# Optimization experiments

Hardware: AMD Instinct MI355X
Metric: run time of the kernel (lower is better)

The kernel has to match this reference:

```python
import jax, jax.numpy as jnp
import numpy as np

# irreps_in = 64x0e + 32x1o + 16x2e ; output of FCTP = 64x0e
MULS = (64, 32, 16)
LS = (0, 1, 2)
IRR_DIM = sum(m * (2 * l + 1) for m, l in zip(MULS, LS))  # 240
HID = 64   # hidden_fea_len
Z = 64     # z_fea_len
N = 50000
# e3nn path normalization ('element', normalization='component'):
# each l x l -> 0e path weight = sqrt(ir_out.dim / sum_paths(mul1*mul2)) = 1/sqrt(64^2+32^2+16^2)
PATH_NORM = 1.0 / np.sqrt(sum(m * m for m in MULS))


def _split(t):
    # slice flat irrep vector into per-irrep [N, mul, 2l+1] blocks
    blocks, i = [], 0
    for m, l in zip(MULS, LS):
        d = 2 * l + 1
        blocks.append(t[:, i:i + m * d].reshape(-1, m, d))
        i += m * d
    return blocks


def _fctp(t, W0, W1, W2):
    # FullyConnectedTensorProduct(irr, irr, '64x0e'):
    # for each l, CG w3j(l,l,0)[m,m'] = delta_{mm'} / sqrt(2l+1),
    # out[n,k] = sum_l pw_l * sum_{u,v} W_l[u,v,k] * <x_l[n,u,:], x_l[n,v,:]> / sqrt(2l+1)
    out = 0.0
    for x, W, l in zip(_split(t), (W0, W1, W2), LS):
        d = 2 * l + 1
        dot = jnp.einsum('num,nvm->nuv', x, x) * (PATH_NORM / np.sqrt(d))
        out = out + jnp.einsum('nuv,uvk->nk', dot, W)
    return out


def _mlp(h, A1, b1, A2, b2, A3, b3):
    h = jax.nn.silu(h @ A1.T + b1)
    h = jax.nn.silu(h @ A2.T + b2)
    return h @ A3.T + b3


def setup_inputs() -> dict:
    key = jax.random.key(0)
    ks = jax.random.split(key, 8)
    return {
        'tensor_in': jax.random.normal(ks[0], (N, IRR_DIM), jnp.float32),
        # FCTP weights (e3nn init: standard normal; normalization lives in PATH_NORM)
        'W0': jax.random.normal(ks[1], (64, 64, HID), jnp.float32),
        'W1': jax.random.normal(ks[2], (32, 32, HID), jnp.float32),
        'W2': jax.random.normal(ks[3], (16, 16, HID), jnp.float32),
        # nn.Linear params (y = x @ A.T + b)
        'A1': jax.random.normal(ks[4], (HID, HID), jnp.float32) / np.sqrt(HID),
        'b1': jnp.zeros((HID,), jnp.float32),
        'A2': jax.random.normal(ks[5], (Z, HID), jnp.float32) / np.sqrt(HID),
        'b2': jnp.zeros((Z,), jnp.float32),
        'A3': jax.random.normal(ks[6], (Z, Z), jnp.float32) / np.sqrt(Z),
        'b3': jnp.zeros((Z,), jnp.float32),
    }


def reference(tensor_in, W0, W1, W2, A1, b1, A2, b2, A3, b3):
    def fwd(t):
        return _mlp(_fctp(t, W0, W1, W2), A1, b1, A2, b2, A3, b3)

    # x = MLP(FCTP(t, t)); y = d(sum(x))/dt  (autograd.grad with ones grad_outputs)
    x, vjp_fn = jax.vjp(fwd, tensor_in)
    y = vjp_fn(jnp.ones_like(x))[0]
    return (x, y)
```

## Files before the change

### kernel.cpp

```cpp
#include <hip/hip_runtime.h>
#include <math.h>
#include <utility>


typedef short bf8 __attribute__((ext_vector_type(8)));
typedef float f4 __attribute__((ext_vector_type(4)));

constexpr int IRR = 240;

constexpr int NP = 2880;

struct PTab { short u[NP]; short v[NP]; signed char l[NP]; };
constexpr PTab build_ptab() {
    PTab t{}; int p = 0;
    for (int u = 0; u < 64; u++) for (int v = u; v < 64; v++) { t.u[p]=(short)u; t.v[p]=(short)v; t.l[p]=0; p++; }
    while (p < 2112) { t.l[p] = -1; p++; }
    for (int u = 0; u < 32; u++) for (int v = u; v < 32; v++) { t.u[p]=(short)u; t.v[p]=(short)v; t.l[p]=1; p++; }
    while (p < 2688) { t.l[p] = -1; p++; }
    for (int u = 0; u < 16; u++) for (int v = u; v < 16; v++) { t.u[p]=(short)u; t.v[p]=(short)v; t.l[p]=2; p++; }
    while (p < NP)   { t.l[p] = -1; p++; }
    return t;
}
constexpr PTab PT = build_ptab();

constexpr size_t B_WTF = 0;
constexpr size_t B_WB  = (size_t)64 * NP * 2;
constexpr size_t B_A1T = B_WB + (size_t)5376 * 64 * 2;
constexpr size_t B_A2T = B_A1T + 16384;
constexpr size_t B_A3T = B_A2T + 16384;
constexpr size_t B_DG2 = B_A3T + 16384;
constexpr size_t B_H   = B_DG2 + 256;

__device__ __forceinline__ unsigned short f2bf(float x) {
    unsigned int u = __float_as_uint(x);
    return (unsigned short)((u + 0x7fffu + ((u >> 16) & 1u)) >> 16);
}
__device__ __forceinline__ unsigned pack2(float a, float b) {
    unsigned ua = __float_as_uint(a) + 0x8000u;
    unsigned ub = __float_as_uint(b) + 0x8000u;
    return __builtin_amdgcn_perm(ub, ua, 0x07060302u);
}

__global__ void prep_kernel(const float* __restrict__ W0, const float* __restrict__ W1,
                            const float* __restrict__ W2, const float* __restrict__ A1,
                            const float* __restrict__ A2, const float* __restrict__ A3,
                            unsigned short* __restrict__ wtf, unsigned short* __restrict__ wb,
                            float* __restrict__ a1t, float* __restrict__ a2t,
                            float* __restrict__ a3t, float* __restrict__ dg2)
{
    int idx = blockIdx.x * blockDim.x + threadIdx.x;
    const double c0 = 1.0 / sqrt(5376.0);
    const double cl_[3] = { c0, c0 / sqrt(3.0), c0 / sqrt(5.0) };
    if (idx < 64 * NP) {
        int c = idx / NP, p = idx - c * NP;
        unsigned short val = 0;
        int l = -1, local = 0, mul = 0;
        if (p < 2112)      { local = p;        if (local < 2080) { l = 0; mul = 64; } }
        else if (p < 2688) { local = p - 2112; if (local < 528)  { l = 1; mul = 32; } }
        else               { local = p - 2688; if (local < 136)  { l = 2; mul = 16; } }
        if (l >= 0) {
            int u = 0;
            while ((u + 1) * mul - (u + 1) * u / 2 <= local) u++;
            int v = u + (local - (u * mul - u * (u - 1) / 2));
            const float* W = (l == 0) ? W0 : (l == 1) ? W1 : W2;
            float wv = W[(u * mul + v) * 64 + c];
            if (u != v) wv += W[(v * mul + u) * 64 + c];
            val = f2bf((float)(cl_[l] * wv));
        }
        wtf[(size_t)c * NP + p] = val;
        return;
    }
    idx -= 64 * NP;
    if (idx < 5376 * 64) {
        int pair = idx >> 6, c = idx & 63;
        int l, w, v, mul;
        if (pair < 4096)      { l = 0; mul = 64; w = pair >> 6;          v = pair & 63; }
        else if (pair < 5120) { l = 1; mul = 32; w = (pair - 4096) >> 5; v = (pair - 4096) & 31; }
        else                  { l = 2; mul = 16; w = (pair - 5120) >> 4; v = (pair - 5120) & 15; }
        const float* W = (l == 0) ? W0 : (l == 1) ? W1 : W2;
        float val;
        if (v == w) val = (float)(2.0 * cl_[l]) * W[(w * mul + w) * 64 + c];
        else        val = (float)cl_[l] * (W[(w * mul + v) * 64 + c] + W[(v * mul + w) * 64 + c]);
        wb[(size_t)pair * 64 + c] = f2bf(val);
        return;
    }
    idx -= 5376 * 64;
    if (idx < 3 * 4096) {
        int m = idx >> 12, e = idx & 4095;
        int j = e >> 6, k = e & 63;
        const float* A = (m == 0) ? A1 : (m == 1) ? A2 : A3;
        float* dst     = (m == 0) ? a1t : (m == 1) ? a2t : a3t;
        dst[j * 64 + k] = A[k * 64 + j];
        return;
    }
    idx -= 3 * 4096;
    if (idx < 64) {
        float s = 0.f;
        for (int k = 0; k < 64; k++) s += A3[k * 64 + idx];
        dg2[idx] = s;
    }
}

template <int P, int NX>
__device__ __forceinline__ float pval(const float (&x)[NX]) {
    constexpr int l = PT.l[P];
    if constexpr (l < 0) {
        return 0.f;
    } else if constexpr (l == 0) {
        return x[PT.u[P]] * x[PT.v[P]];
    } else if constexpr (l == 1) {
        constexpr int u = 3 * PT.u[P], v = 3 * PT.v[P];
        return x[u] * x[v] + x[u + 1] * x[v + 1] + x[u + 2] * x[v + 2];
    } else {
        constexpr int u = 5 * PT.u[P], v = 5 * PT.v[P];
        return x[u] * x[v] + x[u + 1] * x[v + 1] + x[u + 2] * x[v + 2]
             + x[u + 3] * x[v + 3] + x[u + 4] * x[v + 4];
    }
}

template <int CH, int O, int NX>
__device__ __forceinline__ void p_octet(const float (&xr)[NX],
        unsigned short (&Pb)[64][64], int lane)
{
    uint4 w;
    w.x = pack2(pval<CH * 64 + O * 8 + 0, NX>(xr), pval<CH * 64 + O * 8 + 1, NX>(xr));
    w.y = pack2(pval<CH * 64 + O * 8 + 2, NX>(xr), pval<CH * 64 + O * 8 + 3, NX>(xr));
    w.z = pack2(pval<CH * 64 + O * 8 + 4, NX>(xr), pval<CH * 64 + O * 8 + 5, NX>(xr));
    w.w = pack2(pval<CH * 64 + O * 8 + 6, NX>(xr), pval<CH * 64 + O * 8 + 7, NX>(xr));
    *(uint4*)&Pb[lane][(O ^ (lane & 7)) * 8] = w;
}

template <int CH, int NX, int... Os>
__device__ __forceinline__ void p_octets(std::integer_sequence<int, Os...>,
        const float (&xr)[NX], unsigned short (&Pb)[64][64], int lane)
{
    (p_octet<CH, Os, NX>(xr, Pb, lane), ...);
}

template <int CH>
__device__ __forceinline__ void load_bfrags(bf8 (&b)[8],
        const unsigned short* __restrict__ wtf, int l15, int quad)
{
    #pragma unroll
    for (int ct = 0; ct < 4; ++ct)
        #pragma unroll
        for (int ks = 0; ks < 2; ++ks)
            b[ct * 2 + ks] = *(const bf8*)(wtf + (size_t)(16 * ct + l15) * NP
                                           + CH * 64 + ks * 32 + quad * 8);
}

template <int CH, int NX>
__device__ __forceinline__ void fwd_body(const float (&xr)[NX],
        unsigned short (&Pb)[64][64], f4 (&acc)[4][4], const bf8 (&bc)[8],
        int lane, int l15, int quad)
{
    p_octets<CH, NX>(std::make_integer_sequence<int, 8>{}, xr, Pb, lane);
    asm volatile("s_waitcnt lgkmcnt(0)" ::: "memory");
    bf8 a[4][2];
    #pragma unroll
    for (int rt = 0; rt < 4; ++rt) {
        int row = 16 * rt + l15;
        #pragma unroll
        for (int ks = 0; ks < 2; ++ks)
            a[rt][ks] = *(const bf8*)&Pb[row][((ks * 4 + quad) ^ (row & 7)) * 8];
    }
    #pragma unroll
    for (int ct = 0; ct < 4; ++ct)
        #pragma unroll
        for (int ks = 0; ks < 2; ++ks)
            #pragma unroll
            for (int rt = 0; rt < 4; ++rt)
                acc[rt][ct] = __builtin_amdgcn_mfma_f32_16x16x32_bf16(
                                  a[rt][ks], bc[ct * 2 + ks], acc[rt][ct], 0, 0, 0);
    asm volatile("" ::: "memory");
}

template <int B, int N, int I, int NX>
__device__ __forceinline__ void fwd_rec(const float (&xr)[NX],
        unsigned short (&Pb)[64][64], const unsigned short* __restrict__ wtf,
        f4 (&acc)[4][4], bf8 (&bc)[8], int lane, int l15, int quad)
{
    if constexpr (I + 1 < N) {
        bf8 bn[8];
        load_bfrags<B + I + 1>(bn, wtf, l15, quad);
        fwd_body<B + I, NX>(xr, Pb, acc, bc, lane, l15, quad);
        fwd_rec<B, N, I + 1, NX>(xr, Pb, wtf, acc, bn, lane, l15, quad);
    } else {
        fwd_body<B + I, NX>(xr, Pb, acc, bc, lane, l15, quad);
    }
}

template <int B, int N, int NX>
__device__ __forceinline__ void fwd_run_pf(const float (&xr)[NX],
        unsigned short (&Pb)[64][64], const unsigned short* __restrict__ wtf,
        f4 (&acc)[4][4], int lane, int l15, int quad)
{
    bf8 b0[8];
    load_bfrags<B>(b0, wtf, l15, quad);
    fwd_rec<B, N, 0, NX>(xr, Pb, wtf, acc, b0, lane, l15, quad);
}

__global__ __launch_bounds__(256) void fctp_fwd4(const float* __restrict__ tin,
        const unsigned short* __restrict__ wtf, float* __restrict__ h, int n)
{
    __shared__ unsigned short Pb[4][64][64];
    const int tid = threadIdx.x;
    const int wv = tid >> 6;
    const int lane = tid & 63;
    const int l15 = lane & 15, quad = lane >> 4;
    const int s0 = blockIdx.x * 64;
    const int s = s0 + lane;
    const int sld = (s < n) ? s : (n - 1);
    const float* xrow = tin + (size_t)sld * IRR;
    f4 acc[4][4];
    #pragma unroll
    for (int rt = 0; rt < 4; ++rt)
        #pragma unroll
        for (int ct = 0; ct < 4; ++ct) acc[rt][ct] = (f4){0.f, 0.f, 0.f, 0.f};

    if (wv == 0) {
        float x0[64];
        #pragma unroll
        for (int q = 0; q < 16; ++q) *(float4*)&x0[4 * q] = *(const float4*)(xrow + 4 * q);
        fwd_run_pf<0, 17>(x0, Pb[0], wtf, acc, lane, l15, quad);
    } else if (wv == 1) {
        float x0[64];
        #pragma unroll
        for (int q = 0; q < 16; ++q) *(float4*)&x0[4 * q] = *(const float4*)(xrow + 4 * q);
        fwd_run_pf<17, 16>(x0, Pb[1], wtf, acc, lane, l15, quad);
    } else if (wv == 2) {
        float x1[96];
        #pragma unroll
        for (int q = 0; q < 24; ++q) *(float4*)&x1[4 * q] = *(const float4*)(xrow + 64 + 4 * q);
        fwd_run_pf<33, 9>(x1, Pb[2], wtf, acc, lane, l15, quad);
    } else {
        float x2[80];
        #pragma unroll
        for (int q = 0; q < 20; ++q) *(float4*)&x2[4 * q] = *(const float4*)(xrow + 160 + 4 * q);
        fwd_run_pf<42, 3>(x2, Pb[3], wtf, acc, lane, l15, quad);
    }

    float* red = (float*)Pb;
    #pragma unroll
    for (int rt = 0; rt < 4; ++rt) {
        __syncthreads();
        #pragma unroll
        for (int ct = 0; ct < 4; ++ct) {
            float4 v = make_float4(acc[rt][ct][0], acc[rt][ct][1], acc[rt][ct][2], acc[rt][ct][3]);
            *(float4*)&red[(size_t)(wv * 64 + lane) * 20 + ct * 4] = v;
        }
        __syncthreads();
        float4 sum = make_float4(0.f, 0.f, 0.f, 0.f);
        #pragma unroll
        for (int w = 0; w < 4; ++w) {
            float4 v = *(const float4*)&red[(size_t)(w * 64 + lane) * 20 + wv * 4];
            sum.x += v.x; sum.y += v.y; sum.z += v.z; sum.w += v.w;
        }
        #pragma unroll
        for (int r = 0; r < 4; ++r) {
            int row = s0 + 16 * rt + 4 * quad + r;
            if (row < n) h[(size_t)row * 64 + 16 * wv + l15] = (&sum.x)[r];
        }
    }
}

__device__ __forceinline__ void load_awb(int ch, const unsigned short* __restrict__ wb,
        bf8 (&a)[8], int l15, int quad)
{
    #pragma unroll
    for (int rt = 0; rt < 4; ++rt)
        #pragma unroll
        for (int ks = 0; ks < 2; ++ks)
            a[rt * 2 + ks] = *(const bf8*)(wb + (size_t)(ch * 64 + 16 * rt + l15) * 64
                                           + ks * 32 + quad * 8);
}

__device__ __forceinline__ float l0_chunk(const bf8 (&a)[8], const bf8 (&bh)[4][2],
        const float (&xr)[64], int quad)
{
    float p0 = 0.f, p1 = 0.f, p2 = 0.f, p3 = 0.f;
    #pragma unroll
    for (int rt = 0; rt < 4; ++rt) {
        f4 dpR[4];
        #pragma unroll
        for (int ct = 0; ct < 4; ++ct) dpR[ct] = (f4){0.f, 0.f, 0.f, 0.f};
        #pragma unroll
        for (int ks = 0; ks < 2; ++ks)
            #pragma unroll
            for (int ct = 0; ct < 4; ++ct)
                dpR[ct] = __builtin_amdgcn_mfma_f32_16x16x32_bf16(
                              a[rt * 2 + ks], bh[ct][ks], dpR[ct], 0, 0, 0);
        #pragma unroll
        for (int r = 0; r < 4; ++r) {
            p0 += dpR[0][r] * xr[ 0 + rt * 4 + r];
            p1 += dpR[1][r] * xr[16 + rt * 4 + r];
            p2 += dpR[2][r] * xr[32 + rt * 4 + r];
            p3 += dpR[3][r] * xr[48 + rt * 4 + r];
        }
    }
    p0 += __shfl_xor(p0, 16); p0 += __shfl_xor(p0, 32);
    p1 += __shfl_xor(p1, 16); p1 += __shfl_xor(p1, 32);
    p2 += __shfl_xor(p2, 16); p2 += __shfl_xor(p2, 32);
    p3 += __shfl_xor(p3, 16); p3 += __shfl_xor(p3, 32);
    return (quad == 0) ? p0 : (quad == 1) ? p1 : (quad == 2) ? p2 : p3;
}

__global__ __launch_bounds__(256) void fctp_bwd_l0(const float* __restrict__ tin,
        const unsigned short* __restrict__ wb, const float* __restrict__ dh,
        float* __restrict__ y, int n)
{
    __shared__ __align__(16) unsigned char smem[64 * 68 * 4];
    float (*x0t)[68] = (float (*)[68])smem;
    unsigned short (*dhb)[64] = (unsigned short (*)[64])smem;

    const int tid  = threadIdx.x;
    const int wv   = tid >> 6;
    const int lane = tid & 63;
    const int l15 = lane & 15, quad = lane >> 4;
    const int s0 = blockIdx.x * 64;
    const int s = s0 + lane;
    const int sld = (s < n) ? s : (n - 1);
    const bool act = s < n;
    const float* xrow = tin + (size_t)sld * IRR;

    #pragma unroll
    for (int q = 0; q < 4; ++q)
        *(float4*)&x0t[lane][16 * wv + 4 * q] = *(const float4*)(xrow + 16 * wv + 4 * q);
    __syncthreads();
    float xr[64];
    #pragma unroll
    for (int ct = 0; ct < 4; ++ct)
        #pragma unroll
        for (int rt = 0; rt < 4; ++rt)
            *(float4*)&xr[ct * 16 + rt * 4] =
                *(const float4*)&x0t[16 * ct + l15][16 * rt + 4 * quad];
    __syncthreads();
    {
        const float* dhp = dh + (size_t)sld * 64;
        #pragma unroll
        for (int oo = 0; oo < 2; ++oo) {
            int o = 2 * wv + oo;
            float4 f0 = *(const float4*)(dhp + 8 * o);
            float4 f1 = *(const float4*)(dhp + 8 * o + 4);
            uint4 w = make_uint4(pack2(f0.x, f0.y), pack2(f0.z, f0.w),
                                 pack2(f1.x, f1.y), pack2(f1.z, f1.w));
            *(uint4*)&dhb[lane][(o ^ (lane & 7)) * 8] = w;
        }
    }
    __syncthreads();
    bf8 bh[4][2];
    #pragma unroll
    for (int ct = 0; ct < 4; ++ct) {
        int row = 16 * ct + l15;
        #pragma unroll
        for (int ks = 0; ks < 2; ++ks)
            bh[ct][ks] = *(const bf8*)&dhb[row][((ks * 4 + quad) ^ (row & 7)) * 8];
    }

    const int cbase = blockIdx.y * 16 + wv * 4;
    bf8 aA[8], aB[8];
    float res[4];
    load_awb(cbase + 0, wb, aA, l15, quad);
    load_awb(cbase + 1, wb, aB, l15, quad);
    res[0] = l0_chunk(aA, bh, xr, quad);
    load_awb(cbase + 2, wb, aA, l15, quad);
    res[1] = l0_chunk(aB, bh, xr, quad);
    load_awb(cbase + 3, wb, aB, l15, quad);
    res[2] = l0_chunk(aA, bh, xr, quad);
    res[3] = l0_chunk(aB, bh, xr, quad);
    if (act)
        *(float4*)&y[(size_t)s * IRR + cbase] = make_float4(res[0], res[1], res[2], res[3]);
}

__device__ __forceinline__ void bwd_mm(int ch, const unsigned short* __restrict__ wb,
        const bf8 (&bh)[4][2], float (*dPb)[68],
        int lane, int l15, int quad)
{
    f4 dp[4][4];
    #pragma unroll
    for (int rt = 0; rt < 4; ++rt)
        #pragma unroll
        for (int ct = 0; ct < 4; ++ct) dp[rt][ct] = (f4){0.f, 0.f, 0.f, 0.f};
    #pragma unroll
    for (int rt = 0; rt < 4; ++rt) {
        #pragma unroll
        for (int ks = 0; ks < 2; ++ks) {
            bf8 a = *(const bf8*)(wb + (size_t)(ch * 64 + 16 * rt + l15) * 64 + ks * 32 + quad * 8);
            #pragma unroll
            for (int ct = 0; ct < 4; ++ct)
                dp[rt][ct] = __builtin_amdgcn_mfma_f32_16x16x32_bf16(a, bh[ct][ks], dp[rt][ct], 0, 0, 0);
        }
    }
    #pragma unroll
    for (int rt = 0; rt < 4; ++rt)
        #pragma unroll
        for (int ct = 0; ct < 4; ++ct) {
            float4 v = make_float4(dp[rt][ct][0], dp[rt][ct][1], dp[rt][ct][2], dp[rt][ct][3]);
            *(float4*)&dPb[16 * ct + l15][16 * rt + 4 * quad] = v;
        }
    asm volatile("s_waitcnt lgkmcnt(0)" ::: "memory");
}

__global__ __launch_bounds__(256) void fctp_bwd_l12(const float* __restrict__ tin,
        const unsigned short* __restrict__ wb, const float* __restrict__ dh,
        float* __restrict__ y, int n)
{
    __shared__ __align__(16) unsigned char smem[4][64 * 68 * 4];

    const int tid  = threadIdx.x;
    const int wv   = tid >> 6;
    const int lane = tid & 63;
    const int l15 = lane & 15, quad = lane >> 4;
    float (*dPb)[68] = (float (*)[68])smem[wv];
    unsigned short (*dhb)[64] = (unsigned short (*)[64])smem[wv];

    const int sb = blockIdx.x * 4 + wv;
    const int s0 = sb * 64;
    const int s = s0 + lane;
    const int sld = (s < n) ? s : (n - 1);
    const bool act = s < n;
    {
        const float* dhp = dh + (size_t)sld * 64;
        #pragma unroll
        for (int o = 0; o < 8; ++o) {
            float4 f0 = *(const float4*)(dhp + 8 * o);
            float4 f1 = *(const float4*)(dhp + 8 * o + 4);
            uint4 w = make_uint4(pack2(f0.x, f0.y), pack2(f0.z, f0.w),
                                 pack2(f1.x, f1.y), pack2(f1.z, f1.w));
            *(uint4*)&dhb[lane][(o ^ (lane & 7)) * 8] = w;
        }
    }
    asm volatile("s_waitcnt lgkmcnt(0)" ::: "memory");
    bf8 bh[4][2];
    #pragma unroll
    for (int ct = 0; ct < 4; ++ct) {
        int row = 16 * ct + l15;
        #pragma unroll
        for (int ks = 0; ks < 2; ++ks)
            bh[ct][ks] = *(const bf8*)&dhb[row][((ks * 4 + quad) ^ (row & 7)) * 8];
    }
    asm volatile("" ::: "memory");
    const float* xrow = tin + (size_t)sld * IRR;
    float* yrow = y + (size_t)sld * IRR;

    if (blockIdx.y < 2) {
        float x1[96];
        #pragma unroll
        for (int q = 0; q < 24; ++q) *(float4*)&x1[4 * q] = *(const float4*)(xrow + 64 + 4 * q);
        const int cbase = blockIdx.y * 8;
        for (int i = 0; i < 8; ++i) {
            const int c1 = cbase + i;
            bwd_mm(64 + c1, wb, bh, dPb, lane, l15, quad);
            float r[2][3] = {{0.f, 0.f, 0.f}, {0.f, 0.f, 0.f}};
            #pragma unroll
            for (int v = 0; v < 32; v += 4) {
                float4 dA = *(const float4*)&dPb[lane][v];
                float4 dB = *(const float4*)&dPb[lane][32 + v];
                #pragma unroll
                for (int vv = 0; vv < 4; ++vv) {
                    float da = (&dA.x)[vv], db = (&dB.x)[vv];
                    #pragma unroll
                    for (int m = 0; m < 3; ++m) {
                        r[0][m] += da * x1[3 * (v + vv) + m];
                        r[1][m] += db * x1[3 * (v + vv) + m];
                    }
                }
            }
            if (act) {
                #pragma unroll
                for (int wi = 0; wi < 2; ++wi)
                    #pragma unroll
                    for (int m = 0; m < 3; ++m)
                        yrow[64 + (2 * c1 + wi) * 3 + m] = r[wi][m];
            }
        }
    } else {
        float x2[80];
        #pragma unroll
        for (int q = 0; q < 20; ++q) *(float4*)&x2[4 * q] = *(const float4*)(xrow + 160 + 4 * q);
        for (int c2 = 0; c2 < 4; ++c2) {
            bwd_mm(80 + c2, wb, bh, dPb, lane, l15, quad);
            float r[4][5] = {};
            #pragma unroll
            for (int t = 0; t < 4; ++t) {
                #pragma unroll
                for (int v = 0; v < 16; v += 4) {
                    float4 d = *(const float4*)&dPb[lane][t * 16 + v];
                    #pragma unroll
                    for (int vv = 0; vv < 4; ++vv)
                        #pragma unroll
                        for (int m = 0; m < 5; ++m)
                            r[t][m] += (&d.x)[vv] * x2[5 * (v + vv) + m];
                }
            }
            if (act) {
                #pragma unroll
                for (int t = 0; t < 4; ++t)
                    #pragma unroll
                    for (int m = 0; m < 5; ++m)
                        yrow[160 + (4 * c2 + t) * 5 + m] = r[t][m];
            }
        }
    }
}

__global__ __launch_bounds__(256) void mlp4(
    const float* __restrict__ h, const float* __restrict__ A1,
    const float* __restrict__ A2, const float* __restrict__ a1t,
    const float* __restrict__ a2t, const float* __restrict__ a3t,
    const float* __restrict__ b1, const float* __restrict__ b2,
    const float* __restrict__ b3, const float* __restrict__ dg2,
    float* __restrict__ xout, float* __restrict__ dhout, int n)
{
    __shared__ float sact[64][65];
    const int tid  = threadIdx.x;
    const int lane = tid & 63;
    const int ch0  = __builtin_amdgcn_readfirstlane((tid >> 6) * 16);
    const int s    = blockIdx.x * 64 + lane;
    const bool valid = s < n;
    const int sld  = valid ? s : (n - 1);

    {
        const float* hp = h + (size_t)sld * 64 + ch0;
        #pragma unroll
        for (int q = 0; q < 4; ++q) {
            float4 v = *(const float4*)(hp + 4 * q);
            sact[lane][ch0 + 4 * q + 0] = v.x;
            sact[lane][ch0 + 4 * q + 1] = v.y;
            sact[lane][ch0 + 4 * q + 2] = v.z;
            sact[lane][ch0 + 4 * q + 3] = v.w;
        }
    }
    __syncthreads();

    float acc[16], z1[16], z2[16];

    #pragma unroll
    for (int k = 0; k < 16; ++k) acc[k] = b1[ch0 + k];
    #pragma unroll 4
    for (int j = 0; j < 64; ++j) {
        float aj = sact[lane][j];
        const float* r = a1t + j * 64 + ch0;
        #pragma unroll
        for (int k = 0; k < 16; ++k) acc[k] += aj * r[k];
    }
    __syncthreads();
    #pragma unroll
    for (int k = 0; k < 16; ++k) {
        float z = acc[k]; z1[k] = z;
        float sg = 1.f / (1.f + __expf(-z));
        sact[lane][ch0 + k] = z * sg;
    }
    __syncthreads();

    #pragma unroll
    for (int k = 0; k < 16; ++k) acc[k] = b2[ch0 + k];
    #pragma unroll 4
    for (int j = 0; j < 64; ++j) {
        float aj = sact[lane][j];
        const float* r = a2t + j * 64 + ch0;
        #pragma unroll
        for (int k = 0; k < 16; ++k) acc[k] += aj * r[k];
    }
    __syncthreads();
    #pragma unroll
    for (int k = 0; k < 16; ++k) {
        float z = acc[k]; z2[k] = z;
        float sg = 1.f / (1.f + __expf(-z));
        sact[lane][ch0 + k] = z * sg;
    }
    __syncthreads();

    #pragma unroll
    for (int k = 0; k < 16; ++k) acc[k] = b3[ch0 + k];
    #pragma unroll 4
    for (int j = 0; j < 64; ++j) {
        float aj = sact[lane][j];
        const float* r = a3t + j * 64 + ch0;
        #pragma unroll
        for (int k = 0; k < 16; ++k) acc[k] += aj * r[k];
    }
    if (valid) {
        float4* xo = (float4*)(xout + (size_t)s * 64 + ch0);
        #pragma unroll
        for (int q = 0; q < 4; ++q)
            xo[q] = make_float4(acc[4 * q], acc[4 * q + 1], acc[4 * q + 2], acc[4 * q + 3]);
    }

    __syncthreads();
    #pragma unroll
    for (int k = 0; k < 16; ++k) {
        float z = z2[k];
        float sg = 1.f / (1.f + __expf(-z));
        sact[lane][ch0 + k] = dg2[ch0 + k] * sg * (1.f + z * (1.f - sg));
    }
    __syncthreads();

    #pragma unroll
    for (int k = 0; k < 16; ++k) acc[k] = 0.f;
    #pragma unroll 4
    for (int kk = 0; kk < 64; ++kk) {
        float d = sact[lane][kk];
        const float* r = A2 + kk * 64 + ch0;
        #pragma unroll
        for (int k = 0; k < 16; ++k) acc[k] += d * r[k];
    }
    __syncthreads();
    #pragma unroll
    for (int k = 0; k < 16; ++k) {
        float z = z1[k];
        float sg = 1.f / (1.f + __expf(-z));
        sact[lane][ch0 + k] = acc[k] * sg * (1.f + z * (1.f - sg));
    }
    __syncthreads();

    #pragma unroll
    for (int k = 0; k < 16; ++k) acc[k] = 0.f;
    #pragma unroll 4
    for (int j = 0; j < 64; ++j) {
        float d = sact[lane][j];
        const float* r = A1 + j * 64 + ch0;
        #pragma unroll
        for (int k = 0; k < 16; ++k) acc[k] += d * r[k];
    }
    if (valid) {
        float4* dho = (float4*)(dhout + (size_t)s * 64 + ch0);
        #pragma unroll
        for (int q = 0; q < 4; ++q)
            dho[q] = make_float4(acc[4 * q], acc[4 * q + 1], acc[4 * q + 2], acc[4 * q + 3]);
    }
}

extern "C" void kernel_launch(void* const* d_in, const int* in_sizes, int n_in,
                              void* d_out, int out_size, void* d_ws, size_t ws_size,
                              hipStream_t stream)
{
    const float* tin = (const float*)d_in[0];
    const float* W0  = (const float*)d_in[1];
    const float* W1  = (const float*)d_in[2];
    const float* W2  = (const float*)d_in[3];
    const float* A1  = (const float*)d_in[4];
    const float* b1  = (const float*)d_in[5];
    const float* A2  = (const float*)d_in[6];
    const float* b2  = (const float*)d_in[7];
    const float* A3  = (const float*)d_in[8];
    const float* b3  = (const float*)d_in[9];
    float* out = (float*)d_out;
    char* ws   = (char*)d_ws;
    const int n = in_sizes[0] / IRR;

    unsigned short* wtf = (unsigned short*)(ws + B_WTF);
    unsigned short* wb  = (unsigned short*)(ws + B_WB);
    float* a1t  = (float*)(ws + B_A1T);
    float* a2t  = (float*)(ws + B_A2T);
    float* a3t  = (float*)(ws + B_A3T);
    float* dg2  = (float*)(ws + B_DG2);
    float* h    = (float*)(ws + B_H);
    float* dh   = h + (size_t)n * 64;
    float* xout = out;
    float* yout = out + (size_t)n * 64;

    const int total_prep = 64 * NP + 5376 * 64 + 3 * 4096 + 64;
    prep_kernel<<<(total_prep + 255) / 256, 256, 0, stream>>>(W0, W1, W2, A1, A2, A3,
                                                              wtf, wb, a1t, a2t, a3t, dg2);
    const int nb64 = (n + 63) / 64;
    fctp_fwd4<<<nb64, 256, 0, stream>>>(tin, wtf, h, n);
    mlp4<<<nb64, 256, 0, stream>>>(h, A1, A2, a1t, a2t, a3t,
                                   b1, b2, b3, dg2, xout, dh, n);
    fctp_bwd_l0<<<dim3(nb64, 4), 256, 0, stream>>>(tin, wb, dh, yout, n);
    fctp_bwd_l12<<<dim3((nb64 + 3) / 4, 3), 256, 0, stream>>>(tin, wb, dh, yout, n);
}
```

Before: 329.4 us.

## Split FCTP forward pair-blocks across four grid slices with partial-sum reduction in MLP

The forward tensor-product kernel is split along a new grid dimension into four slices, each handling a balanced subset of the 45 pair blocks. Each slice writes its own partial h buffer, and the MLP kernel sums the four partials when loading h. The aim is more parallelism and better load balance, since the original per-wave work was uneven (17/16/9/3 blocks). In exchange, input rows are read redundantly across slices and h traffic rises fourfold. The path is used only when the workspace is large enough, otherwise the old single-slice launch runs.

```diff
diff --git a/kernel.cpp b/kernel.cpp
--- a/kernel.cpp
+++ b/kernel.cpp
@@ -200,6 +200,20 @@
     fwd_rec<B, N, 0, NX>(xr, Pb, wtf, acc, b0, lane, l15, quad);
 }
 
+__device__ __forceinline__ void load_x0(float (&x0)[64], const float* xrow) {
+    #pragma unroll
+    for (int q = 0; q < 16; ++q) *(float4*)&x0[4 * q] = *(const float4*)(xrow + 4 * q);
+}
+__device__ __forceinline__ void load_x1(float (&x1)[96], const float* xrow) {
+    #pragma unroll
+    for (int q = 0; q < 24; ++q) *(float4*)&x1[4 * q] = *(const float4*)(xrow + 64 + 4 * q);
+}
+__device__ __forceinline__ void load_x2(float (&x2)[80], const float* xrow) {
+    #pragma unroll
+    for (int q = 0; q < 20; ++q) *(float4*)&x2[4 * q] = *(const float4*)(xrow + 160 + 4 * q);
+}
+
+template <int SPLIT>
 __global__ __launch_bounds__(256) void fctp_fwd4(const float* __restrict__ tin,
         const unsigned short* __restrict__ wtf, float* __restrict__ h, int n)
 {
@@ -212,32 +226,41 @@
     const int s = s0 + lane;
     const int sld = (s < n) ? s : (n - 1);
     const float* xrow = tin + (size_t)sld * IRR;
+    float* hout = h + (SPLIT == 4 ? (size_t)blockIdx.y * ((size_t)n * 64) : (size_t)0);
     f4 acc[4][4];
     #pragma unroll
     for (int rt = 0; rt < 4; ++rt)
         #pragma unroll
         for (int ct = 0; ct < 4; ++ct) acc[rt][ct] = (f4){0.f, 0.f, 0.f, 0.f};
 
-    if (wv == 0) {
-        float x0[64];
-        #pragma unroll
-        for (int q = 0; q < 16; ++q) *(float4*)&x0[4 * q] = *(const float4*)(xrow + 4 * q);
-        fwd_run_pf<0, 17>(x0, Pb[0], wtf, acc, lane, l15, quad);
-    } else if (wv == 1) {
-        float x0[64];
-        #pragma unroll
-        for (int q = 0; q < 16; ++q) *(float4*)&x0[4 * q] = *(const float4*)(xrow + 4 * q);
-        fwd_run_pf<17, 16>(x0, Pb[1], wtf, acc, lane, l15, quad);
-    } else if (wv == 2) {
-        float x1[96];
-        #pragma unroll
-        for (int q = 0; q < 24; ++q) *(float4*)&x1[4 * q] = *(const float4*)(xrow + 64 + 4 * q);
-        fwd_run_pf<33, 9>(x1, Pb[2], wtf, acc, lane, l15, quad);
+    if constexpr (SPLIT == 1) {
+        if (wv == 0)      { float x0[64]; load_x0(x0, xrow); fwd_run_pf< 0, 17>(x0, Pb[0], wtf, acc, lane, l15, quad); }
+        else if (wv == 1) { float x0[64]; load_x0(x0, xrow); fwd_run_pf<17, 16>(x0, Pb[1], wtf, acc, lane, l15, quad); }
+        else if (wv == 2) { float x1[96]; load_x1(x1, xrow); fwd_run_pf<33,  9>(x1, Pb[2], wtf, acc, lane, l15, quad); }
+        else              { float x2[80]; load_x2(x2, xrow); fwd_run_pf<42,  3>(x2, Pb[3], wtf, acc, lane, l15, quad); }
     } else {
-        float x2[80];
-        #pragma unroll
-        for (int q = 0; q < 20; ++q) *(float4*)&x2[4 * q] = *(const float4*)(xrow + 160 + 4 * q);
-        fwd_run_pf<42, 3>(x2, Pb[3], wtf, acc, lane, l15, quad);
+        const int yb = blockIdx.y;
+        if (yb == 0) {
+            if (wv == 0)      { float x0[64]; load_x0(x0, xrow); fwd_run_pf< 0, 4>(x0, Pb[0], wtf, acc, lane, l15, quad); }
+            else if (wv == 1) { float x0[64]; load_x0(x0, xrow); fwd_run_pf< 4, 4>(x0, Pb[1], wtf, acc, lane, l15, quad); }
+            else if (wv == 2) { float x0[64]; load_x0(x0, xrow); fwd_run_pf< 8, 3>(x0, Pb[2], wtf, acc, lane, l15, quad); }
+            else              { float x0[64]; load_x0(x0, xrow); fwd_run_pf<11, 2>(x0, Pb[3], wtf, acc, lane, l15, quad); }
+        } else if (yb == 1) {
+            if (wv == 0)      { float x0[64]; load_x0(x0, xrow); fwd_run_pf<13, 4>(x0, Pb[0], wtf, acc, lane, l15, quad); }
+            else if (wv == 1) { float x0[64]; load_x0(x0, xrow); fwd_run_pf<17, 4>(x0, Pb[1], wtf, acc, lane, l15, quad); }
+            else if (wv == 2) { float x0[64]; load_x0(x0, xrow); fwd_run_pf<21, 3>(x0, Pb[2], wtf, acc, lane, l15, quad); }
+            else              { float x0[64]; load_x0(x0, xrow); fwd_run_pf<24, 2>(x0, Pb[3], wtf, acc, lane, l15, quad); }
+        } else if (yb == 2) {
+            if (wv == 0)      { float x0[64]; load_x0(x0, xrow); fwd_run_pf<26, 4>(x0, Pb[0], wtf, acc, lane, l15, quad); }
+            else if (wv == 1) { float x0[64]; load_x0(x0, xrow); fwd_run_pf<30, 3>(x0, Pb[1], wtf, acc, lane, l15, quad); }
+            else if (wv == 2) { float x1[96]; load_x1(x1, xrow); fwd_run_pf<33, 2>(x1, Pb[2], wtf, acc, lane, l15, quad); }
+            else              { float x1[96]; load_x1(x1, xrow); fwd_run_pf<35, 2>(x1, Pb[3], wtf, acc, lane, l15, quad); }
+        } else {
+            if (wv == 0)      { float x1[96]; load_x1(x1, xrow); fwd_run_pf<37, 3>(x1, Pb[0], wtf, acc, lane, l15, quad); }
+            else if (wv == 1) { float x1[96]; load_x1(x1, xrow); fwd_run_pf<40, 2>(x1, Pb[1], wtf, acc, lane, l15, quad); }
+            else if (wv == 2) { float x2[80]; load_x2(x2, xrow); fwd_run_pf<42, 1>(x2, Pb[2], wtf, acc, lane, l15, quad); }
+            else              { float x2[80]; load_x2(x2, xrow); fwd_run_pf<43, 2>(x2, Pb[3], wtf, acc, lane, l15, quad); }
+        }
     }
 
     float* red = (float*)Pb;
@@ -259,7 +282,7 @@
         #pragma unroll
         for (int r = 0; r < 4; ++r) {
             int row = s0 + 16 * rt + 4 * quad + r;
-            if (row < n) h[(size_t)row * 64 + 16 * wv + l15] = (&sum.x)[r];
+            if (row < n) hout[(size_t)row * 64 + 16 * wv + l15] = (&sum.x)[r];
         }
     }
 }
@@ -504,6 +527,7 @@
     }
 }
 
+template <int NS>
 __global__ __launch_bounds__(256) void mlp4(
     const float* __restrict__ h, const float* __restrict__ A1,
     const float* __restrict__ A2, const float* __restrict__ a1t,
@@ -519,12 +543,18 @@
     const int s    = blockIdx.x * 64 + lane;
     const bool valid = s < n;
     const int sld  = valid ? s : (n - 1);
+    const size_t sstr = (size_t)n * 64;
 
     {
         const float* hp = h + (size_t)sld * 64 + ch0;
         #pragma unroll
         for (int q = 0; q < 4; ++q) {
             float4 v = *(const float4*)(hp + 4 * q);
+            #pragma unroll
+            for (int sl = 1; sl < NS; ++sl) {
+                float4 w = *(const float4*)(hp + sl * sstr + 4 * q);
+                v.x += w.x; v.y += w.y; v.z += w.z; v.w += w.w;
+            }
             sact[lane][ch0 + 4 * q + 0] = v.x;
             sact[lane][ch0 + 4 * q + 1] = v.y;
             sact[lane][ch0 + 4 * q + 2] = v.z;
@@ -655,18 +685,28 @@
     float* a2t  = (float*)(ws + B_A2T);
     float* a3t  = (float*)(ws + B_A3T);
     float* dg2  = (float*)(ws + B_DG2);
-    float* h    = (float*)(ws + B_H);
-    float* dh   = h + (size_t)n * 64;
+    float* hp   = (float*)(ws + B_H);
+
+    const size_t sstr = (size_t)n * 64;
+    const bool wide = ws_size >= B_H + 5 * sstr * sizeof(float);
+    const int ns = wide ? 4 : 1;
+    float* dh   = hp + (size_t)ns * sstr;
     float* xout = out;
-    float* yout = out + (size_t)n * 64;
+    float* yout = out + sstr;
 
     const int total_prep = 64 * NP + 5376 * 64 + 3 * 4096 + 64;
     prep_kernel<<<(total_prep + 255) / 256, 256, 0, stream>>>(W0, W1, W2, A1, A2, A3,
                                                               wtf, wb, a1t, a2t, a3t, dg2);
     const int nb64 = (n + 63) / 64;
-    fctp_fwd4<<<nb64, 256, 0, stream>>>(tin, wtf, h, n);
-    mlp4<<<nb64, 256, 0, stream>>>(h, A1, A2, a1t, a2t, a3t,
-                                   b1, b2, b3, dg2, xout, dh, n);
+    if (wide) {
+        fctp_fwd4<4><<<dim3(nb64, 4), 256, 0, stream>>>(tin, wtf, hp, n);
+        mlp4<4><<<nb64, 256, 0, stream>>>(hp, A1, A2, a1t, a2t, a3t,
+                                          b1, b2, b3, dg2, xout, dh, n);
+    } else {
+        fctp_fwd4<1><<<nb64, 256, 0, stream>>>(tin, wtf, hp, n);
+        mlp4<1><<<nb64, 256, 0, stream>>>(hp, A1, A2, a1t, a2t, a3t,
+                                          b1, b2, b3, dg2, xout, dh, n);
+    }
     fctp_bwd_l0<<<dim3(nb64, 4), 256, 0, stream>>>(tin, wb, dh, yout, n);
     fctp_bwd_l12<<<dim3((nb64 + 3) / 4, 3), 256, 0, stream>>>(tin, wb, dh, yout, n);
 }
```

Measured after the change: 363.0 us. +10.2%, slower.
